# Performance work log

Measured on AMD Instinct MI355X. Metric: run time of the kernel, lower is better.

## Reference

```python
import jax, jax.numpy as jnp
import numpy as np

B, S, E, H, D = 4, 2048, 2048, 16, 128
EPS = 1e-6


def _rope_cache(seq_len, dim, base=10000.0):
    # standard rotary cache, half-split layout matching rotate_half
    inv_freq = 1.0 / (base ** (np.arange(0, dim // 2, dtype=np.float32) / (dim // 2)))
    t = np.arange(seq_len, dtype=np.float32)
    freqs = np.outer(t, inv_freq)                     # [S, D/2]
    emb = np.concatenate([freqs, freqs], axis=-1)     # [S, D]
    cos = jnp.asarray(np.cos(emb))[None, :, None, :]  # [1, S, 1, D]
    sin = jnp.asarray(np.sin(emb))[None, :, None, :]
    return cos, sin


def setup_inputs() -> dict:
    key = jax.random.key(0)
    ks = jax.random.split(key, 5)
    scale = 1.0 / np.sqrt(E)
    x = jax.random.normal(ks[0], (B, S, E), dtype=jnp.float32)
    Wq = jax.random.normal(ks[1], (E, E), dtype=jnp.float32) * scale
    Wk = jax.random.normal(ks[2], (E, E), dtype=jnp.float32) * scale
    Wv = jax.random.normal(ks[3], (E, E), dtype=jnp.float32) * scale
    Wo = jax.random.normal(ks[4], (E, E), dtype=jnp.float32) * scale
    cos, sin = _rope_cache(S, D)
    return {"x": x, "cos": cos, "sin": sin, "Wq": Wq, "Wk": Wk, "Wv": Wv, "Wo": Wo}


def _rotate_half(t):
    d = t.shape[-1] // 2
    return jnp.concatenate([-t[..., d:], t[..., :d]], axis=-1)


def _rms_norm(t, eps):
    return t * jax.lax.rsqrt(jnp.mean(t * t, axis=-1, keepdims=True) + eps)


def reference(x, cos, sin, Wq, Wk, Wv, Wo):
    b, s, _ = x.shape
    # QKV projections (Linear without bias: x @ W.T), reshape to heads
    q = (x @ Wq.T).reshape(b, s, H, D)
    k = (x @ Wk.T).reshape(b, s, H, D)
    v = (x @ Wv.T).reshape(b, s, H, D)
    # RoPE then QK RMSNorm (no learned scale)
    q = _rms_norm(q * cos + _rotate_half(q) * sin, EPS)
    k = _rms_norm(k * cos + _rotate_half(k) * sin, EPS)
    # non-causal SDPA
    scores = jnp.einsum("bqhd,bkhd->bhqk", q, k) / np.sqrt(D)
    probs = jax.nn.softmax(scores, axis=-1)
    y = jnp.einsum("bhqk,bkhd->bqhd", probs, v).reshape(b, s, H * D)
    return y @ Wo.T
```

## Files before the change

### kernel.cpp

```cpp
#include <hip/hip_runtime.h>
#include <hip/hip_bf16.h>
#include <math.h>


typedef __bf16 bf16_t;
typedef __bf16 bf16x2 __attribute__((ext_vector_type(2)));
typedef __bf16 bf16x4 __attribute__((ext_vector_type(4)));
typedef __bf16 bf16x8 __attribute__((ext_vector_type(8)));
typedef float f32x2 __attribute__((ext_vector_type(2)));
typedef float f32x4 __attribute__((ext_vector_type(4)));
typedef float f32x16 __attribute__((ext_vector_type(16)));
typedef unsigned int u32;
typedef u32 u32x4 __attribute__((ext_vector_type(4)));

typedef __attribute__((address_space(1))) const void gas_cvoid;
typedef __attribute__((address_space(3))) void las_void;

#define MFMA16(a, b, c) __builtin_amdgcn_mfma_f32_16x16x32_bf16((a), (b), (c), 0, 0, 0)
#define MFMA32(a, b, c) __builtin_amdgcn_mfma_f32_32x32x16_bf16((a), (b), (c), 0, 0, 0)

__device__ __forceinline__ void gload16(const void* g, void* l) {
  __builtin_amdgcn_global_load_lds((gas_cvoid*)g, (las_void*)l, 16, 0, 0);
}
__device__ __forceinline__ void pl32(u32& a, u32& b) {
  asm volatile("v_permlane32_swap_b32 %0, %1" : "+v"(a), "+v"(b));
}
__device__ __forceinline__ float fexp2(float x) {
  float r;
  asm("v_exp_f32 %0, %1" : "=v"(r) : "v"(x));
  return r;
}

__global__ __launch_bounds__(256) void cvt_all(const float* __restrict__ x,
                                               const float* __restrict__ w0,
                                               const float* __restrict__ w1,
                                               const float* __restrict__ w2,
                                               const float* __restrict__ w3,
                                               bf16_t* __restrict__ xo,
                                               bf16_t* __restrict__ o0,
                                               bf16_t* __restrict__ o1,
                                               bf16_t* __restrict__ o2,
                                               bf16_t* __restrict__ o3) {
  const float* in;
  bf16_t* out;
  size_t i;
  if (blockIdx.x < 16384) {
    in = x; out = xo;
    i = ((size_t)blockIdx.x * 256 + threadIdx.x) * 4;
  } else {
    const int which = (blockIdx.x - 16384) >> 12;
    in = which == 0 ? w0 : which == 1 ? w1 : which == 2 ? w2 : w3;
    out = which == 0 ? o0 : which == 1 ? o1 : which == 2 ? o2 : o3;
    i = ((size_t)((blockIdx.x - 16384) & 4095) * 256 + threadIdx.x) * 4;
  }
  f32x4 v = *(const f32x4*)&in[i];
  bf16x4 o;
#pragma unroll
  for (int j = 0; j < 4; ++j) o[j] = (bf16_t)v[j];
  *(bf16x4*)&out[i] = o;
}

template <int MODE, typename CT, int NT_T>
__global__ __launch_bounds__(512, 2) void gemm8(const bf16_t* __restrict__ A,
                                                const bf16_t* __restrict__ Bt,
                                                CT* __restrict__ C,
                                                const float* __restrict__ Cs,
                                                const float* __restrict__ Sn) {
  constexpr int K = 2048;
  __shared__ __attribute__((aligned(16))) char lds[131072];
  const int tid = threadIdx.x;
  const int wave = tid >> 6, lane = tid & 63;
  const int bid = blockIdx.x;
  const int swz = (bid & 7) * 32 + (bid >> 3);
  const int m0 = (swz / NT_T) * 256, n0 = (swz % NT_T) * 256;

  const int srow = tid >> 3;
  const int scol = ((tid & 7) ^ (srow & 7)) * 8;
  const bf16_t* aBase = A + (size_t)(m0 + srow) * K + scol;
  const bf16_t* bBase = Bt + (size_t)(n0 + srow) * K + scol;

  const int wm = wave >> 2, wn = wave & 3;
  const int l15 = lane & 15, l4 = lane >> 4;
  const int axor = l15 & 7;
  char* const wdst = lds + wave * 1024;

  f32x4 acc[8][4] = {};

  gload16(bBase, wdst + 32768);
  gload16(bBase + (size_t)64 * K, wdst + 32768 + 8192);
  gload16(bBase + (size_t)128 * K, wdst + 32768 + 16384);
  gload16(bBase + (size_t)192 * K, wdst + 32768 + 24576);
  gload16(aBase, wdst);
  gload16(aBase + (size_t)128 * K, wdst + 16384);
  gload16(aBase + (size_t)64 * K, wdst + 8192);
  gload16(aBase + (size_t)192 * K, wdst + 24576);

  for (int t = 0; t < 32; ++t) {
    const int buf = t & 1, nbuf = buf ^ 1;
    const char* la = lds + buf * 65536 + wm * 16384;
    const char* lb = lds + buf * 65536 + 32768 + (wn >> 1) * 16384 + (wn & 1) * 8192;
    char* const ndst = wdst + nbuf * 65536;
    bf16x8 bF[4][2];
#pragma unroll
    for (int q = 0; q < 4; ++q) {
      if (q == 0) {
        asm volatile("s_waitcnt vmcnt(2)" ::: "memory");
      } else if (q == 2) {
        if (t < 31)
          asm volatile("s_waitcnt vmcnt(4)" ::: "memory");
        else
          asm volatile("s_waitcnt vmcnt(0)" ::: "memory");
      }
      __builtin_amdgcn_s_barrier();

      bf16x8 aF[2][2];
#pragma unroll
      for (int dm = 0; dm < 2; ++dm)
#pragma unroll
        for (int kk = 0; kk < 2; ++kk)
          aF[dm][kk] = *(const bf16x8*)(la + ((q * 2 + dm) * 16 + l15) * 128 +
                                        ((kk * 4 + l4) ^ axor) * 16);
      if (q == 0) {
#pragma unroll
        for (int ni = 0; ni < 4; ++ni)
#pragma unroll
          for (int kk = 0; kk < 2; ++kk)
            bF[ni][kk] = *(const bf16x8*)(lb + (ni * 16 + l15) * 128 +
                                          ((kk * 4 + l4) ^ axor) * 16);
      }
      if (t < 31) {
        const int off = (t + 1) * 64;
        if (q == 0) {
          gload16(bBase + off, ndst + 32768);
          gload16(bBase + (size_t)64 * K + off, ndst + 32768 + 8192);
        } else if (q == 1) {
          gload16(bBase + (size_t)128 * K + off, ndst + 32768 + 16384);
          gload16(bBase + (size_t)192 * K + off, ndst + 32768 + 24576);
        } else if (q == 2) {
          gload16(aBase + off, ndst);
          gload16(aBase + (size_t)128 * K + off, ndst + 16384);
        } else {
          gload16(aBase + (size_t)64 * K + off, ndst + 8192);
          gload16(aBase + (size_t)192 * K + off, ndst + 24576);
        }
      }
      __builtin_amdgcn_s_setprio(1);
#pragma unroll
      for (int kk = 0; kk < 2; ++kk)
#pragma unroll
        for (int dm = 0; dm < 2; ++dm)
#pragma unroll
          for (int ni = 0; ni < 4; ++ni)
            acc[q * 2 + dm][ni] = MFMA16(aF[dm][kk], bF[ni][kk], acc[q * 2 + dm][ni]);
      __builtin_amdgcn_s_setprio(0);
    }
  }

  if (MODE == 3) {
    __syncthreads();
    bf16_t* ct = (bf16_t*)lds;
    const int lrow0 = wm * 128 + l4 * 4;
    const int lcol0 = wn * 64 + l15;
#pragma unroll
    for (int mi = 0; mi < 8; ++mi)
#pragma unroll
      for (int ni = 0; ni < 4; ++ni)
#pragma unroll
        for (int j = 0; j < 4; ++j)
          ct[(lrow0 + mi * 16 + j) * 256 + lcol0 + ni * 16] = (bf16_t)acc[mi][ni][j];
    __syncthreads();
#pragma unroll 1
    for (int it = 0; it < 64; ++it) {
      const int item = wave * 64 + it;
      const int lr = item >> 1, hl = item & 1;
      const int r = m0 + lr;
      const int s = r & 2047, b = r >> 11;
      const int hh = (n0 >> 7) + hl;
      const u32 qw = *(const u32*)&ct[lr * 256 + hl * 128 + 2 * lane];
      const bf16x2 qv = __builtin_bit_cast(bf16x2, qw);
      const float a0 = (float)qv[0], a1 = (float)qv[1];
      f32x2 cv = *(const f32x2*)&Cs[(size_t)s * 128 + 2 * lane];
      f32x2 sv = *(const f32x2*)&Sn[(size_t)s * 128 + 2 * lane];
      const float p0 = __shfl_xor(a0, 32);
      const float p1 = __shfl_xor(a1, 32);
      const float sg = (lane < 32) ? -1.f : 1.f;
      const float r0 = a0 * cv.x + sg * p0 * sv.x;
      const float r1 = a1 * cv.y + sg * p1 * sv.y;
      float ss = r0 * r0 + r1 * r1;
#pragma unroll
      for (int off = 1; off < 64; off <<= 1) ss += __shfl_xor(ss, off);
      const float inv = rsqrtf(ss * (1.0f / 128.0f) + 1e-6f);
      bf16x2 o;
      o[0] = (bf16_t)(r0 * inv);
      o[1] = (bf16_t)(r1 * inv);
      *(bf16x2*)&((bf16_t*)C)[(((size_t)(b * 16 + hh)) * 2048 + s) * 128 + 2 * lane] = o;
    }
    return;
  }

  const int rBase = m0 + wm * 128 + l4 * 4;
  const int cBase = n0 + wn * 64 + l15;
#pragma unroll
  for (int mi = 0; mi < 8; ++mi)
#pragma unroll
    for (int ni = 0; ni < 4; ++ni)
#pragma unroll
      for (int j = 0; j < 4; ++j) {
        const int r = rBase + mi * 16 + j;
        const int c = cBase + ni * 16;
        const CT v = (CT)acc[mi][ni][j];
        if (MODE == 0) {
          const int b = r >> 11, s = r & 2047, hh = c >> 7, d = c & 127;
          C[(((size_t)(b * 16 + hh)) * 2048 + s) * 128 + d] = v;
        } else if (MODE == 1) {
          C[(size_t)r * 2048 + c] = v;
        } else {
          const int hh = r >> 7, dd = r & 127, b = c >> 11, s = c & 2047;
          C[((size_t)(b * 16 + hh) * 128 + dd) * 2048 + s] = v;
        }
      }
}

__global__ __launch_bounds__(512, 2) void attn_fwd(const bf16_t* __restrict__ Q,
                                                   const bf16_t* __restrict__ K,
                                                   const bf16_t* __restrict__ Vt,
                                                   bf16_t* __restrict__ Y) {
  __shared__ __attribute__((aligned(16))) bf16_t ldsK[2][64 * 128];
  __shared__ __attribute__((aligned(16))) bf16_t ldsV[2][128 * 64];
  const int tid = threadIdx.x, wave = tid >> 6, lane = tid & 63;
  const int l31 = lane & 31, hi = lane >> 5;
  const int pid = blockIdx.x;
  const int bh = (pid & 7) * 8 + ((pid >> 3) & 7);
  const int qb = pid >> 6;
  const int b = bh >> 4, h = bh & 15;
  const bf16_t* Qh = Q + (size_t)bh * 2048 * 128;
  const bf16_t* Kh = K + (size_t)bh * 2048 * 128;
  const bf16_t* Vh = Vt + (size_t)bh * 128 * 2048;
  const int q0 = qb * 256 + wave * 32;

  bf16x8 qf[8];
#pragma unroll
  for (int dk = 0; dk < 8; ++dk)
    qf[dk] = *(const bf16x8*)&Qh[(size_t)(q0 + l31) * 128 + dk * 16 + hi * 8];

  f32x16 ot[4] = {};
  float l_r = 0.f;
  const float SC2 = 0.08838834764831845f * 1.44269504088896341f;
  const float NC2 = -11.5f * 1.44269504088896341f;

  auto stage = [&](int kt, int bu) {
#pragma unroll
    for (int i = 0; i < 2; ++i) {
      const int G = wave * 64 + lane + i * 512;
      char* dstK = (char*)&ldsK[bu][0] + (wave * 64 + i * 512) * 16;
      char* dstV = (char*)&ldsV[bu][0] + (wave * 64 + i * 512) * 16;
      const int kvr = G >> 4, glk = G & 15;
      gload16(Kh + (size_t)(kt * 64 + kvr) * 128 + ((glk ^ (kvr & 7)) * 8), dstK);
      const int dr = G >> 3, glv = G & 7;
      gload16(Vh + (size_t)dr * 2048 + kt * 64 + ((glv ^ (dr & 7)) * 8), dstV);
    }
  };

  stage(0, 0);
  stage(1, 1);
  asm volatile("s_waitcnt vmcnt(4)" ::: "memory");
  __builtin_amdgcn_s_barrier();
  __builtin_amdgcn_sched_barrier(0);

  for (int kt = 0; kt < 32; ++kt) {
    const int bu = kt & 1;
    const int r7 = l31 & 7;

    f32x16 sa0 = {}, sa1 = {};
    __builtin_amdgcn_s_setprio(1);
#pragma unroll
    for (int dk = 0; dk < 8; ++dk) {
      const int g = ((dk << 1) | hi) ^ r7;
      bf16x8 kf0 = *(const bf16x8*)&ldsK[bu][l31 * 128 + g * 8];
      bf16x8 kf1 = *(const bf16x8*)&ldsK[bu][(32 + l31) * 128 + g * 8];
      sa0 = MFMA32(kf0, qf[dk], sa0);
      sa1 = MFMA32(kf1, qf[dk], sa1);
    }
    __builtin_amdgcn_s_setprio(0);

    u32 w[2][8];
    float ssum = 0.f;
#pragma unroll
    for (int i = 0; i < 8; ++i) {
      const float p0 = fexp2(fmaf(sa0[2 * i], SC2, NC2));
      const float p1 = fexp2(fmaf(sa0[2 * i + 1], SC2, NC2));
      const float p2 = fexp2(fmaf(sa1[2 * i], SC2, NC2));
      const float p3 = fexp2(fmaf(sa1[2 * i + 1], SC2, NC2));
      ssum += (p0 + p1) + (p2 + p3);
      bf16x2 t0, t1;
      t0[0] = (bf16_t)p0; t0[1] = (bf16_t)p1;
      t1[0] = (bf16_t)p2; t1[1] = (bf16_t)p3;
      w[0][i] = __builtin_bit_cast(u32, t0);
      w[1][i] = __builtin_bit_cast(u32, t1);
    }
    ssum += __shfl_xor(ssum, 32);
    l_r += ssum;

#pragma unroll
    for (int ks = 0; ks < 4; ++ks) {
      const int tsel = ks >> 1, k4 = (ks & 1) * 4;
      u32 a0 = w[tsel][k4 + 0], b0 = w[tsel][k4 + 2];
      u32 a1 = w[tsel][k4 + 1], b1 = w[tsel][k4 + 3];
      pl32(a0, b0);
      pl32(a1, b1);
      u32x4 fw;
      fw.x = a0; fw.y = a1; fw.z = b0; fw.w = b1;
      const bf16x8 pf = __builtin_bit_cast(bf16x8, fw);
      const int gv = ((ks << 1) | hi) ^ r7;
      __builtin_amdgcn_s_setprio(1);
#pragma unroll
      for (int db = 0; db < 4; ++db) {
        bf16x8 vf = *(const bf16x8*)&ldsV[bu][(db * 32 + l31) * 64 + gv * 8];
        ot[db] = MFMA32(vf, pf, ot[db]);
      }
      __builtin_amdgcn_s_setprio(0);
    }

    __builtin_amdgcn_s_barrier();
    __builtin_amdgcn_sched_barrier(0);
    if (kt < 30) {
      stage(kt + 2, bu);
      asm volatile("s_waitcnt vmcnt(4)" ::: "memory");
    } else {
      asm volatile("s_waitcnt vmcnt(0)" ::: "memory");
    }
    __builtin_amdgcn_s_barrier();
    __builtin_amdgcn_sched_barrier(0);
  }

  const float rl = 1.f / l_r;
  const size_t yrow = ((size_t)(b * 2048 + q0 + l31) * 16 + h) * 128;
#pragma unroll
  for (int db = 0; db < 4; ++db)
#pragma unroll
    for (int g2 = 0; g2 < 4; ++g2) {
      bf16x4 ov;
#pragma unroll
      for (int j = 0; j < 4; ++j) ov[j] = (bf16_t)(ot[db][g2 * 4 + j] * rl);
      *(bf16x4*)&Y[yrow + db * 32 + g2 * 8 + hi * 4] = ov;
    }
}

extern "C" void kernel_launch(void* const* d_in, const int* in_sizes, int n_in,
                              void* d_out, int out_size, void* d_ws, size_t ws_size,
                              hipStream_t stream) {
  const float* x = (const float*)d_in[0];
  const float* cs = (const float*)d_in[1];
  const float* sn = (const float*)d_in[2];
  const float* Wq = (const float*)d_in[3];
  const float* Wk = (const float*)d_in[4];
  const float* Wv = (const float*)d_in[5];
  const float* Wo = (const float*)d_in[6];

  bf16_t* ws = (bf16_t*)d_ws;
  const size_t TSZ = (size_t)4 * 2048 * 2048;
  const size_t WSZ = (size_t)2048 * 2048;
  bf16_t* xb = ws;
  bf16_t* Wqb = ws + TSZ;
  bf16_t* Wkb = Wqb + WSZ;
  bf16_t* Wvb = Wkb + WSZ;
  bf16_t* Wob = Wvb + WSZ;
  bf16_t* Qb = ws + 2 * TSZ;
  bf16_t* Kb = Qb + TSZ;
  bf16_t* Vtb = Kb + TSZ;
  bf16_t* Yb = xb;

  cvt_all<<<32768, 256, 0, stream>>>(x, Wq, Wk, Wv, Wo, xb, Wqb, Wkb, Wvb, Wob);

  gemm8<3, bf16_t, 8><<<256, 512, 0, stream>>>(xb, Wqb, Qb, cs, sn);
  gemm8<3, bf16_t, 8><<<256, 512, 0, stream>>>(xb, Wkb, Kb, cs, sn);
  gemm8<2, bf16_t, 32><<<256, 512, 0, stream>>>(Wvb, xb, Vtb, nullptr, nullptr);
  attn_fwd<<<512, 512, 0, stream>>>(Qb, Kb, Vtb, Yb);
  gemm8<1, float, 8><<<256, 512, 0, stream>>>(Yb, Wob, (float*)d_out, nullptr, nullptr);
}
```

Measured before the change: 498.1 us.

## Merge Q/K/V projections into one launch and split RoPE+RMSNorm into separate kernel

Replaces three separate 256-block projection GEMM launches with a single 768-block launch that picks its weight, output and layout by block segment. This gives one fuller wave of work across the CUs and removes launch gaps and tail effects. The fused RoPE/RMSNorm epilogue is moved out of the GEMM into a standalone kernel that reads and rewrites Q and K in place. That costs an extra round trip of Q and K through memory, and the scattered per-element stores now sit in the merged GEMM's epilogue.

Result: faster. 470.9 us (median of 2 runs) (-5.5%).

```diff
diff --git a/kernel.cpp b/kernel.cpp
--- a/kernel.cpp
+++ b/kernel.cpp
@@ -60,19 +60,25 @@
   *(bf16x4*)&out[i] = o;
 }
 
-template <int MODE, typename CT, int NT_T>
-__global__ __launch_bounds__(512, 2) void gemm8(const bf16_t* __restrict__ A,
-                                                const bf16_t* __restrict__ Bt,
-                                                CT* __restrict__ C,
-                                                const float* __restrict__ Cs,
-                                                const float* __restrict__ Sn) {
+__global__ __launch_bounds__(512, 2) void gemm_qkv(const bf16_t* __restrict__ xb,
+                                                   const bf16_t* __restrict__ Wq,
+                                                   const bf16_t* __restrict__ Wk,
+                                                   const bf16_t* __restrict__ Wv,
+                                                   bf16_t* __restrict__ Qo,
+                                                   bf16_t* __restrict__ Ko,
+                                                   bf16_t* __restrict__ Vo) {
   constexpr int K = 2048;
   __shared__ __attribute__((aligned(16))) char lds[131072];
   const int tid = threadIdx.x;
   const int wave = tid >> 6, lane = tid & 63;
-  const int bid = blockIdx.x;
-  const int swz = (bid & 7) * 32 + (bid >> 3);
-  const int m0 = (swz / NT_T) * 256, n0 = (swz % NT_T) * 256;
+  const int seg = blockIdx.x >> 8;
+  const int sbid = blockIdx.x & 255;
+  const int swz = (sbid & 7) * 32 + (sbid >> 3);
+  const int NT = (seg == 2) ? 32 : 8;
+  const int m0 = (swz / NT) * 256, n0 = (swz % NT) * 256;
+  const bf16_t* A = (seg == 2) ? Wv : xb;
+  const bf16_t* Bt = (seg == 0) ? Wq : (seg == 1) ? Wk : xb;
+  bf16_t* C = (seg == 0) ? Qo : (seg == 1) ? Ko : Vo;
 
   const int srow = tid >> 3;
   const int scol = ((tid & 7) ^ (srow & 7)) * 8;
@@ -156,48 +162,6 @@
     }
   }
 
-  if (MODE == 3) {
-    __syncthreads();
-    bf16_t* ct = (bf16_t*)lds;
-    const int lrow0 = wm * 128 + l4 * 4;
-    const int lcol0 = wn * 64 + l15;
-#pragma unroll
-    for (int mi = 0; mi < 8; ++mi)
-#pragma unroll
-      for (int ni = 0; ni < 4; ++ni)
-#pragma unroll
-        for (int j = 0; j < 4; ++j)
-          ct[(lrow0 + mi * 16 + j) * 256 + lcol0 + ni * 16] = (bf16_t)acc[mi][ni][j];
-    __syncthreads();
-#pragma unroll 1
-    for (int it = 0; it < 64; ++it) {
-      const int item = wave * 64 + it;
-      const int lr = item >> 1, hl = item & 1;
-      const int r = m0 + lr;
-      const int s = r & 2047, b = r >> 11;
-      const int hh = (n0 >> 7) + hl;
-      const u32 qw = *(const u32*)&ct[lr * 256 + hl * 128 + 2 * lane];
-      const bf16x2 qv = __builtin_bit_cast(bf16x2, qw);
-      const float a0 = (float)qv[0], a1 = (float)qv[1];
-      f32x2 cv = *(const f32x2*)&Cs[(size_t)s * 128 + 2 * lane];
-      f32x2 sv = *(const f32x2*)&Sn[(size_t)s * 128 + 2 * lane];
-      const float p0 = __shfl_xor(a0, 32);
-      const float p1 = __shfl_xor(a1, 32);
-      const float sg = (lane < 32) ? -1.f : 1.f;
-      const float r0 = a0 * cv.x + sg * p0 * sv.x;
-      const float r1 = a1 * cv.y + sg * p1 * sv.y;
-      float ss = r0 * r0 + r1 * r1;
-#pragma unroll
-      for (int off = 1; off < 64; off <<= 1) ss += __shfl_xor(ss, off);
-      const float inv = rsqrtf(ss * (1.0f / 128.0f) + 1e-6f);
-      bf16x2 o;
-      o[0] = (bf16_t)(r0 * inv);
-      o[1] = (bf16_t)(r1 * inv);
-      *(bf16x2*)&((bf16_t*)C)[(((size_t)(b * 16 + hh)) * 2048 + s) * 128 + 2 * lane] = o;
-    }
-    return;
-  }
-
   const int rBase = m0 + wm * 128 + l4 * 4;
   const int cBase = n0 + wn * 64 + l15;
 #pragma unroll
@@ -208,17 +172,148 @@
       for (int j = 0; j < 4; ++j) {
         const int r = rBase + mi * 16 + j;
         const int c = cBase + ni * 16;
-        const CT v = (CT)acc[mi][ni][j];
-        if (MODE == 0) {
+        const bf16_t v = (bf16_t)acc[mi][ni][j];
+        if (seg < 2) {
           const int b = r >> 11, s = r & 2047, hh = c >> 7, d = c & 127;
           C[(((size_t)(b * 16 + hh)) * 2048 + s) * 128 + d] = v;
-        } else if (MODE == 1) {
-          C[(size_t)r * 2048 + c] = v;
         } else {
           const int hh = r >> 7, dd = r & 127, b = c >> 11, s = c & 2047;
           C[((size_t)(b * 16 + hh) * 128 + dd) * 2048 + s] = v;
         }
       }
+}
+
+__global__ __launch_bounds__(512, 2) void gemm_out(const bf16_t* __restrict__ A,
+                                                   const bf16_t* __restrict__ Bt,
+                                                   float* __restrict__ C) {
+  constexpr int K = 2048;
+  __shared__ __attribute__((aligned(16))) char lds[131072];
+  const int tid = threadIdx.x;
+  const int wave = tid >> 6, lane = tid & 63;
+  const int bid = blockIdx.x;
+  const int swz = (bid & 7) * 32 + (bid >> 3);
+  const int m0 = (swz / 8) * 256, n0 = (swz % 8) * 256;
+
+  const int srow = tid >> 3;
+  const int scol = ((tid & 7) ^ (srow & 7)) * 8;
+  const bf16_t* aBase = A + (size_t)(m0 + srow) * K + scol;
+  const bf16_t* bBase = Bt + (size_t)(n0 + srow) * K + scol;
+
+  const int wm = wave >> 2, wn = wave & 3;
+  const int l15 = lane & 15, l4 = lane >> 4;
+  const int axor = l15 & 7;
+  char* const wdst = lds + wave * 1024;
+
+  f32x4 acc[8][4] = {};
+
+  gload16(bBase, wdst + 32768);
+  gload16(bBase + (size_t)64 * K, wdst + 32768 + 8192);
+  gload16(bBase + (size_t)128 * K, wdst + 32768 + 16384);
+  gload16(bBase + (size_t)192 * K, wdst + 32768 + 24576);
+  gload16(aBase, wdst);
+  gload16(aBase + (size_t)128 * K, wdst + 16384);
+  gload16(aBase + (size_t)64 * K, wdst + 8192);
+  gload16(aBase + (size_t)192 * K, wdst + 24576);
+
+  for (int t = 0; t < 32; ++t) {
+    const int buf = t & 1, nbuf = buf ^ 1;
+    const char* la = lds + buf * 65536 + wm * 16384;
+    const char* lb = lds + buf * 65536 + 32768 + (wn >> 1) * 16384 + (wn & 1) * 8192;
+    char* const ndst = wdst + nbuf * 65536;
+    bf16x8 bF[4][2];
+#pragma unroll
+    for (int q = 0; q < 4; ++q) {
+      if (q == 0) {
+        asm volatile("s_waitcnt vmcnt(2)" ::: "memory");
+      } else if (q == 2) {
+        if (t < 31)
+          asm volatile("s_waitcnt vmcnt(4)" ::: "memory");
+        else
+          asm volatile("s_waitcnt vmcnt(0)" ::: "memory");
+      }
+      __builtin_amdgcn_s_barrier();
+
+      bf16x8 aF[2][2];
+#pragma unroll
+      for (int dm = 0; dm < 2; ++dm)
+#pragma unroll
+        for (int kk = 0; kk < 2; ++kk)
+          aF[dm][kk] = *(const bf16x8*)(la + ((q * 2 + dm) * 16 + l15) * 128 +
+                                        ((kk * 4 + l4) ^ axor) * 16);
+      if (q == 0) {
+#pragma unroll
+        for (int ni = 0; ni < 4; ++ni)
+#pragma unroll
+          for (int kk = 0; kk < 2; ++kk)
+            bF[ni][kk] = *(const bf16x8*)(lb + (ni * 16 + l15) * 128 +
+                                          ((kk * 4 + l4) ^ axor) * 16);
+      }
+      if (t < 31) {
+        const int off = (t + 1) * 64;
+        if (q == 0) {
+          gload16(bBase + off, ndst + 32768);
+          gload16(bBase + (size_t)64 * K + off, ndst + 32768 + 8192);
+        } else if (q == 1) {
+          gload16(bBase + (size_t)128 * K + off, ndst + 32768 + 16384);
+          gload16(bBase + (size_t)192 * K + off, ndst + 32768 + 24576);
+        } else if (q == 2) {
+          gload16(aBase + off, ndst);
+          gload16(aBase + (size_t)128 * K + off, ndst + 16384);
+        } else {
+          gload16(aBase + (size_t)64 * K + off, ndst + 8192);
+          gload16(aBase + (size_t)192 * K + off, ndst + 24576);
+        }
+      }
+      __builtin_amdgcn_s_setprio(1);
+#pragma unroll
+      for (int kk = 0; kk < 2; ++kk)
+#pragma unroll
+        for (int dm = 0; dm < 2; ++dm)
+#pragma unroll
+          for (int ni = 0; ni < 4; ++ni)
+            acc[q * 2 + dm][ni] = MFMA16(aF[dm][kk], bF[ni][kk], acc[q * 2 + dm][ni]);
+      __builtin_amdgcn_s_setprio(0);
+    }
+  }
+
+  const int rBase = m0 + wm * 128 + l4 * 4;
+  const int cBase = n0 + wn * 64 + l15;
+#pragma unroll
+  for (int mi = 0; mi < 8; ++mi)
+#pragma unroll
+    for (int ni = 0; ni < 4; ++ni)
+#pragma unroll
+      for (int j = 0; j < 4; ++j)
+        C[(size_t)(rBase + mi * 16 + j) * 2048 + cBase + ni * 16] = acc[mi][ni][j];
+}
+
+__global__ __launch_bounds__(256) void rope_rms2(bf16_t* __restrict__ Qb,
+                                                 bf16_t* __restrict__ Kb,
+                                                 const float* __restrict__ Cs,
+                                                 const float* __restrict__ Sn) {
+  bf16_t* T = (blockIdx.x >> 12) ? Kb : Qb;
+  const int bid = blockIdx.x & 4095;
+  const int wave = threadIdx.x >> 6, lane = threadIdx.x & 63;
+#pragma unroll 1
+  for (int rr = 0; rr < 8; ++rr) {
+    const size_t row = (size_t)bid * 32 + wave * 8 + rr;
+    const int s = (int)(row & 2047);
+    bf16_t* p = &T[row * 128 + 2 * lane];
+    const float a0 = (float)p[0], a1 = (float)p[1];
+    f32x2 cv = *(const f32x2*)&Cs[(size_t)s * 128 + 2 * lane];
+    f32x2 sv = *(const f32x2*)&Sn[(size_t)s * 128 + 2 * lane];
+    const float p0 = __shfl_xor(a0, 32);
+    const float p1 = __shfl_xor(a1, 32);
+    const float sg = (lane < 32) ? -1.f : 1.f;
+    const float r0 = a0 * cv.x + sg * p0 * sv.x;
+    const float r1 = a1 * cv.y + sg * p1 * sv.y;
+    float ss = r0 * r0 + r1 * r1;
+#pragma unroll
+    for (int off = 1; off < 64; off <<= 1) ss += __shfl_xor(ss, off);
+    const float inv = rsqrtf(ss * (1.0f / 128.0f) + 1e-6f);
+    p[0] = (bf16_t)(r0 * inv);
+    p[1] = (bf16_t)(r1 * inv);
+  }
 }
 
 __global__ __launch_bounds__(512, 2) void attn_fwd(const bf16_t* __restrict__ Q,
@@ -371,10 +466,8 @@
   bf16_t* Yb = xb;
 
   cvt_all<<<32768, 256, 0, stream>>>(x, Wq, Wk, Wv, Wo, xb, Wqb, Wkb, Wvb, Wob);
-
-  gemm8<3, bf16_t, 8><<<256, 512, 0, stream>>>(xb, Wqb, Qb, cs, sn);
-  gemm8<3, bf16_t, 8><<<256, 512, 0, stream>>>(xb, Wkb, Kb, cs, sn);
-  gemm8<2, bf16_t, 32><<<256, 512, 0, stream>>>(Wvb, xb, Vtb, nullptr, nullptr);
+  gemm_qkv<<<768, 512, 0, stream>>>(xb, Wqb, Wkb, Wvb, Qb, Kb, Vtb);
+  rope_rms2<<<8192, 256, 0, stream>>>(Qb, Kb, cs, sn);
   attn_fwd<<<512, 512, 0, stream>>>(Qb, Kb, Vtb, Yb);
-  gemm8<1, float, 8><<<256, 512, 0, stream>>>(Yb, Wob, (float*)d_out, nullptr, nullptr);
-}
+  gemm_out<<<256, 512, 0, stream>>>(Yb, Wob, (float*)d_out);
+}
```
